# Kernel tuning notes

Measured on AMD Instinct MI355X. Metric: run time of the kernel, lower is better.

Reference implementation:

```python
import jax, jax.numpy as jnp
import numpy as np

B, I, O, K = 16384, 512, 64, 4


def setup_inputs() -> dict:
    key = jax.random.key(0)
    k1, k2, k3 = jax.random.split(key, 3)
    x = jax.random.normal(k1, (B, I), dtype=jnp.float32)
    weights = jax.random.normal(k2, (O, I), dtype=jnp.float32)
    # per-(o,i) Fourier coefficients, init like torch.randn * 0.1
    coefficients = jax.random.normal(k3, (O, I, 2 * K + 1), dtype=jnp.float32) * 0.1
    return {"x": x, "weights": weights, "coefficients": coefficients}


def reference(x, weights, coefficients):
    # x: [B, I]; weights: [O, I]; coefficients: [O, I, 2K+1]
    Kf = coefficients.shape[-1] // 2
    freqs = jnp.arange(1, Kf + 1, dtype=x.dtype)          # (k+1) for k in range(K)
    ang = x[:, :, None] * freqs                            # [B, I, K]
    sin_v = jnp.sin(ang)                                   # [B, I, K]
    cos_v = jnp.cos(ang)                                   # [B, I, K]
    c0 = coefficients[..., 0]                              # [O, I] constant term
    a = coefficients[..., 1::2]                            # [O, I, K] sin coeffs
    b = coefficients[..., 2::2]                            # [O, I, K] cos coeffs
    # out[b,o] = sum_i w[o,i] * (c0[o,i] + sum_k a*sin + b*cos)
    const = jnp.sum(weights * c0, axis=1)                  # [O]
    out = (const[None, :]
           + jnp.einsum('bik,oik->bo', sin_v, weights[:, :, None] * a)
           + jnp.einsum('bik,oik->bo', cos_v, weights[:, :, None] * b))
    return out
```

## Files before the change

kernel.cpp:

```cpp
#include <hip/hip_runtime.h>

#define B_ROWS 16384
#define I_DIM  512
#define O_DIM  64
#define NFEAT  8
#define XPAD   516
#define W2_BYTES ((size_t)I_DIM * O_DIM * NFEAT * 2)

typedef _Float16 f16x8 __attribute__((ext_vector_type(8)));
typedef float    f32x4 __attribute__((ext_vector_type(4)));

__global__ __launch_bounds__(256) void prep_w2(const float* __restrict__ w,
                                               const float* __restrict__ coef,
                                               _Float16* __restrict__ w2) {
    int t = blockIdx.x * 256 + threadIdx.x;
    int o = t >> 9;
    int i = t & 511;
    float wv = w[t];
    const float* cp = coef + (size_t)t * 9;
    f16x8 v;
#pragma unroll
    for (int f = 0; f < 8; ++f) v[f] = (_Float16)(wv * cp[f + 1]);
    *reinterpret_cast<f16x8*>(w2 + ((size_t)(i * 64 + o)) * 8) = v;
}

__global__ __launch_bounds__(256) void prep_const(const float* __restrict__ w,
                                                  const float* __restrict__ coef,
                                                  float* __restrict__ cst) {
    int o = blockIdx.x;
    int t = threadIdx.x;
    float s = 0.f;
#pragma unroll
    for (int i = t; i < I_DIM; i += 256)
        s += w[o * I_DIM + i] * coef[((size_t)(o * I_DIM + i)) * 9];
#pragma unroll
    for (int off = 32; off; off >>= 1) s += __shfl_down(s, off, 64);
    __shared__ float ps[4];
    if ((t & 63) == 0) ps[t >> 6] = s;
    __syncthreads();
    if (t == 0) cst[o] = ps[0] + ps[1] + ps[2] + ps[3];
}

__global__ __launch_bounds__(512)
__attribute__((amdgpu_waves_per_eu(2, 2)))
void fourier_main(const float* __restrict__ x,
                  const _Float16* __restrict__ w2,
                  const float* __restrict__ cst,
                  float* __restrict__ out) {
    __shared__ __align__(16) float xs[64][XPAD];
    float (*red)[64][65] = reinterpret_cast<float(*)[64][65]>(&xs[0][0]);

    const int tid   = threadIdx.x;
    const int wave  = tid >> 6;
    const int lane  = tid & 63;
    const int col16 = lane & 15;
    const int ig    = lane >> 4;
    const int rbase = blockIdx.x * 64;
    const int i0    = wave * 64;

    {
        const float4* xg = reinterpret_cast<const float4*>(x + (size_t)rbase * I_DIM);
#pragma unroll
        for (int j = 0; j < 16; ++j) {
            int f4   = j * 512 + tid;
            float4 v = xg[f4];
            *reinterpret_cast<float4*>(&xs[f4 >> 7][(f4 & 127) << 2]) = v;
        }
    }
    __syncthreads();

    f32x4 acc[4][4] = {};
    const f16x8* __restrict__ bbase = reinterpret_cast<const f16x8*>(w2);

    f16x8 bf[4], bn[4];
    {
        const int i = i0 + ig;
#pragma unroll
        for (int n = 0; n < 4; ++n) bf[n] = bbase[i * 64 + n * 16 + col16];
    }

    for (int s = 0; s < 16; ++s) {
        const int i = i0 + s * 4 + ig;

        if (s < 15) {
            const int i2 = i + 4;
#pragma unroll
            for (int n = 0; n < 4; ++n) bn[n] = bbase[i2 * 64 + n * 16 + col16];
        }

        float xv[4];
#pragma unroll
        for (int m = 0; m < 4; ++m) xv[m] = xs[m * 16 + col16][i];

#pragma unroll
        for (int m = 0; m < 4; ++m) {
            float s1, c1;
            __sincosf(xv[m], &s1, &c1);
            const float tc = 2.f * c1;
            const float s2 = tc * s1;
            const float c2 = tc * c1 - 1.f;
            const float s3 = tc * s2 - s1;
            const float c3 = tc * c2 - c1;
            const float s4 = tc * s3 - s2;
            const float c4 = tc * c3 - c2;
            f16x8 af;
            af[0] = (_Float16)s1; af[1] = (_Float16)c1;
            af[2] = (_Float16)s2; af[3] = (_Float16)c2;
            af[4] = (_Float16)s3; af[5] = (_Float16)c3;
            af[6] = (_Float16)s4; af[7] = (_Float16)c4;
#pragma unroll
            for (int n = 0; n < 4; ++n)
                acc[m][n] = __builtin_amdgcn_mfma_f32_16x16x32_f16(af, bf[n], acc[m][n], 0, 0, 0);
        }

#pragma unroll
        for (int n = 0; n < 4; ++n) bf[n] = bn[n];
    }

    __syncthreads();
    if (wave < 4) {
#pragma unroll
        for (int m = 0; m < 4; ++m)
#pragma unroll
            for (int n = 0; n < 4; ++n)
#pragma unroll
                for (int q = 0; q < 4; ++q)
                    red[wave][m * 16 + ig * 4 + q][n * 16 + col16] = acc[m][n][q];
    }
    __syncthreads();
    if (wave >= 4) {
#pragma unroll
        for (int m = 0; m < 4; ++m)
#pragma unroll
            for (int n = 0; n < 4; ++n)
#pragma unroll
                for (int q = 0; q < 4; ++q)
                    red[wave - 4][m * 16 + ig * 4 + q][n * 16 + col16] += acc[m][n][q];
    }
    __syncthreads();

    const float cv = cst[lane];
#pragma unroll
    for (int j = 0; j < 8; ++j) {
        const int r = wave + 8 * j;
        float v = cv + red[0][r][lane] + red[1][r][lane] + red[2][r][lane] + red[3][r][lane];
        out[(size_t)(rbase + r) * 64 + lane] = v;
    }
}

extern "C" void kernel_launch(void* const* d_in, const int* in_sizes, int n_in,
                              void* d_out, int out_size, void* d_ws, size_t ws_size,
                              hipStream_t stream) {
    const float* x    = (const float*)d_in[0];
    const float* w    = (const float*)d_in[1];
    const float* coef = (const float*)d_in[2];
    _Float16* w2  = (_Float16*)d_ws;
    float*    cst = (float*)((char*)d_ws + W2_BYTES);
    float*    out = (float*)d_out;

    hipLaunchKernelGGL(prep_w2,    dim3(128), dim3(256), 0, stream, w, coef, w2);
    hipLaunchKernelGGL(prep_const, dim3(64),  dim3(256), 0, stream, w, coef, cst);
    hipLaunchKernelGGL(fourier_main, dim3(B_ROWS / 64), dim3(512), 0, stream, x, w2, cst, out);
}
```

Measured before the change: 93.24 us.

## Halve row tile, raise occupancy, fuse prep kernels, use native sin/cos

Fuses the two preparation kernels into one launch that computes the f16 weighted coefficients and the constant term together. The main kernel drops from 64 to 32 rows per block, halving accumulators and LDS so each EU can hold four waves instead of two, and launches twice as many blocks. The sin/cos path now scales by 1/(2π), takes the fractional part and calls the hardware sin/cos builtins directly. The trade-off is that each block reloads the full weight matrix for fewer rows, doubling weight traffic per output.

```diff
diff --git a/kernel.cpp b/kernel.cpp
--- a/kernel.cpp
+++ b/kernel.cpp
@@ -4,64 +4,61 @@
 #define I_DIM  512
 #define O_DIM  64
 #define NFEAT  8
+#define TROWS  32
 #define XPAD   516
 #define W2_BYTES ((size_t)I_DIM * O_DIM * NFEAT * 2)
 
 typedef _Float16 f16x8 __attribute__((ext_vector_type(8)));
 typedef float    f32x4 __attribute__((ext_vector_type(4)));
 
-__global__ __launch_bounds__(256) void prep_w2(const float* __restrict__ w,
-                                               const float* __restrict__ coef,
-                                               _Float16* __restrict__ w2) {
-    int t = blockIdx.x * 256 + threadIdx.x;
-    int o = t >> 9;
-    int i = t & 511;
-    float wv = w[t];
-    const float* cp = coef + (size_t)t * 9;
-    f16x8 v;
+__global__ __launch_bounds__(256) void prep(const float* __restrict__ w,
+                                            const float* __restrict__ coef,
+                                            _Float16* __restrict__ w2,
+                                            float* __restrict__ cst) {
+    const int o = blockIdx.x;
+    const int t = threadIdx.x;
+    float csum = 0.f;
 #pragma unroll
-    for (int f = 0; f < 8; ++f) v[f] = (_Float16)(wv * cp[f + 1]);
-    *reinterpret_cast<f16x8*>(w2 + ((size_t)(i * 64 + o)) * 8) = v;
-}
-
-__global__ __launch_bounds__(256) void prep_const(const float* __restrict__ w,
-                                                  const float* __restrict__ coef,
-                                                  float* __restrict__ cst) {
-    int o = blockIdx.x;
-    int t = threadIdx.x;
-    float s = 0.f;
+    for (int ii = 0; ii < 2; ++ii) {
+        const int i   = ii * 256 + t;
+        const int idx = o * I_DIM + i;
+        const float wv = w[idx];
+        const float* cp = coef + (size_t)idx * 9;
+        csum += wv * cp[0];
+        f16x8 v;
 #pragma unroll
-    for (int i = t; i < I_DIM; i += 256)
-        s += w[o * I_DIM + i] * coef[((size_t)(o * I_DIM + i)) * 9];
+        for (int f = 0; f < 8; ++f) v[f] = (_Float16)(wv * cp[f + 1]);
+        *reinterpret_cast<f16x8*>(w2 + ((size_t)(i * 64 + o)) * 8) = v;
+    }
 #pragma unroll
-    for (int off = 32; off; off >>= 1) s += __shfl_down(s, off, 64);
+    for (int off = 32; off; off >>= 1) csum += __shfl_down(csum, off, 64);
     __shared__ float ps[4];
-    if ((t & 63) == 0) ps[t >> 6] = s;
+    if ((t & 63) == 0) ps[t >> 6] = csum;
     __syncthreads();
     if (t == 0) cst[o] = ps[0] + ps[1] + ps[2] + ps[3];
 }
 
 __global__ __launch_bounds__(512)
-__attribute__((amdgpu_waves_per_eu(2, 2)))
+__attribute__((amdgpu_waves_per_eu(4, 4)))
 void fourier_main(const float* __restrict__ x,
                   const _Float16* __restrict__ w2,
                   const float* __restrict__ cst,
                   float* __restrict__ out) {
-    __shared__ __align__(16) float xs[64][XPAD];
-    float (*red)[64][65] = reinterpret_cast<float(*)[64][65]>(&xs[0][0]);
+    __shared__ __align__(16) float xs[TROWS][XPAD];
+    float (*red)[TROWS][65] = reinterpret_cast<float(*)[TROWS][65]>(&xs[0][0]);
 
     const int tid   = threadIdx.x;
     const int wave  = tid >> 6;
     const int lane  = tid & 63;
     const int col16 = lane & 15;
     const int ig    = lane >> 4;
-    const int rbase = blockIdx.x * 64;
+    const int rbase = blockIdx.x * TROWS;
     const int i0    = wave * 64;
 
     {
         const float4* xg = reinterpret_cast<const float4*>(x + (size_t)rbase * I_DIM);
 #pragma unroll
-        for (int j = 0; j < 16; ++j) {
+        for (int j = 0; j < 8; ++j) {
             int f4   = j * 512 + tid;
             float4 v = xg[f4];
             *reinterpret_cast<float4*>(&xs[f4 >> 7][(f4 & 127) << 2]) = v;
@@ -69,8 +66,9 @@
     }
     __syncthreads();
 
-    f32x4 acc[4][4] = {};
+    f32x4 acc[2][4] = {};
     const f16x8* __restrict__ bbase = reinterpret_cast<const f16x8*>(w2);
+    const float RINV = 0.15915494309189535f;
 
     f16x8 bf[4], bn[4];
     {
@@ -88,14 +86,15 @@
             for (int n = 0; n < 4; ++n) bn[n] = bbase[i2 * 64 + n * 16 + col16];
         }
 
-        float xv[4];
+        float xv[2];
 #pragma unroll
-        for (int m = 0; m < 4; ++m) xv[m] = xs[m * 16 + col16][i];
+        for (int m = 0; m < 2; ++m) xv[m] = xs[m * 16 + col16][i];
 
 #pragma unroll
-        for (int m = 0; m < 4; ++m) {
-            float s1, c1;
-            __sincosf(xv[m], &s1, &c1);
+        for (int m = 0; m < 2; ++m) {
+            const float r  = __builtin_amdgcn_fractf(xv[m] * RINV);
+            const float s1 = __builtin_amdgcn_sinf(r);
+            const float c1 = __builtin_amdgcn_cosf(r);
             const float tc = 2.f * c1;
             const float s2 = tc * s1;
             const float c2 = tc * c1 - 1.f;
@@ -120,7 +119,7 @@
     __syncthreads();
     if (wave < 4) {
 #pragma unroll
-        for (int m = 0; m < 4; ++m)
+        for (int m = 0; m < 2; ++m)
 #pragma unroll
             for (int n = 0; n < 4; ++n)
 #pragma unroll
@@ -130,7 +129,7 @@
     __syncthreads();
     if (wave >= 4) {
 #pragma unroll
-        for (int m = 0; m < 4; ++m)
+        for (int m = 0; m < 2; ++m)
 #pragma unroll
             for (int n = 0; n < 4; ++n)
 #pragma unroll
@@ -141,7 +140,7 @@
 
     const float cv = cst[lane];
 #pragma unroll
-    for (int j = 0; j < 8; ++j) {
+    for (int j = 0; j < 4; ++j) {
         const int r = wave + 8 * j;
         float v = cv + red[0][r][lane] + red[1][r][lane] + red[2][r][lane] + red[3][r][lane];
         out[(size_t)(rbase + r) * 64 + lane] = v;
@@ -158,7 +157,6 @@
     float*    cst = (float*)((char*)d_ws + W2_BYTES);
     float*    out = (float*)d_out;
 
-    hipLaunchKernelGGL(prep_w2,    dim3(128), dim3(256), 0, stream, w, coef, w2);
-    hipLaunchKernelGGL(prep_const, dim3(64),  dim3(256), 0, stream, w, coef, cst);
-    hipLaunchKernelGGL(fourier_main, dim3(B_ROWS / 64), dim3(512), 0, stream, x, w2, cst, out);
+    hipLaunchKernelGGL(prep, dim3(O_DIM), dim3(256), 0, stream, w, coef, w2, cst);
+    hipLaunchKernelGGL(fourier_main, dim3(B_ROWS / TROWS), dim3(512), 0, stream, x, w2, cst, out);
 }
```

Measured after the change: 90.28 us. 1.03x faster.
